# Performance work log

Measured on AMD Instinct MI355X. Metric: run time of the kernel, lower is better.

The kernel has to match this reference:

```python
import jax, jax.numpy as jnp
import numpy as np

HIDDEN = 1024
HEADS = 16
BATCH = 2
SEQ = 2048
# dropout_p = 0.1 but module evaluated in eval mode (training=False) -> identity


def setup_inputs() -> dict:
    key = jax.random.key(0)
    k1, k2, k3 = jax.random.split(key, 3)
    x = jax.random.normal(k1, (BATCH, SEQ, HIDDEN), dtype=jnp.float32)
    # unit-scaling Linear: weight ~ N(0,1) (reset_parameters uses nn.init.normal_)
    w_qkv = jax.random.normal(k2, (3 * HIDDEN, HIDDEN), dtype=jnp.float32)
    w_o = jax.random.normal(k3, (HIDDEN, HIDDEN), dtype=jnp.float32)
    return {"x": x, "w_qkv": w_qkv, "w_o": w_o}


def reference(x, w_qkv, w_o):
    b, s, hid = x.shape
    heads = HEADS
    d = hid // heads
    # unit-scaled linear (constraint='to_output_scale'): y = x @ W.T * fan_in**-0.5
    qkv = (x @ w_qkv.T) * (hid ** -0.5)            # [b, s, 3*hid]
    # einops 'b s (z h d) -> z b h s d'
    qkv = qkv.reshape(b, s, 3, heads, d)
    q = jnp.transpose(qkv[:, :, 0], (0, 2, 1, 3))   # [b, h, s, d]
    k = jnp.transpose(qkv[:, :, 1], (0, 2, 1, 3))
    v = jnp.transpose(qkv[:, :, 2], (0, 2, 1, 3))
    # unit-scaled matmul: scale = inner_dim**-0.5
    scores = jnp.einsum('bhqd,bhkd->bhqk', q, k) * (d ** -0.5)  # [b, h, s, s]
    # unit-scaled softmax: output_scale = n / sqrt(n - 1)
    attn = jax.nn.softmax(scores, axis=-1) * (s / np.sqrt(s - 1.0))
    # dropout inactive (eval mode)
    out = jnp.einsum('bhqk,bhkd->bhqd', attn, v) * (s ** -0.5)  # inner dim = s
    out = jnp.transpose(out, (0, 2, 1, 3)).reshape(b, s, hid)   # 'b h s d -> b s (h d)'
    return (out @ w_o.T) * (hid ** -0.5)
```

## Files before the change

### kernel.cpp

```cpp
#include <hip/hip_runtime.h>

typedef unsigned short u16;
typedef _Float16 f16x8 __attribute__((ext_vector_type(8)));
typedef _Float16 f16x4 __attribute__((ext_vector_type(4)));
typedef _Float16 f16x2 __attribute__((ext_vector_type(2)));
typedef float f32x4 __attribute__((ext_vector_type(4)));
typedef unsigned short u16x4 __attribute__((ext_vector_type(4)));

#define HID 1024
#define SEQ 2048
#define NH 16
#define DH 64

__device__ __forceinline__ u16 f2h(float f) {
  return __builtin_bit_cast(u16, (_Float16)f);
}
__device__ __forceinline__ f32x4 mfma_h(f16x8 a, f16x8 b, f32x4 c) {
  return __builtin_amdgcn_mfma_f32_16x16x32_f16(a, b, c, 0, 0, 0);
}
__device__ __forceinline__ float fexp2(float x) {
#if __has_builtin(__builtin_amdgcn_exp2f)
  return __builtin_amdgcn_exp2f(x);
#else
  return __expf(0.69314718f * x);
#endif
}
__device__ __forceinline__ f16x2 pkrtz(float a, float b) {
  return __builtin_bit_cast(f16x2, __builtin_amdgcn_cvt_pkrtz(a, b));
}
__device__ __forceinline__ void g2l16(const u16* g, u16* l) {
  __builtin_amdgcn_global_load_lds(
      (const __attribute__((address_space(1))) unsigned int*)g,
      (__attribute__((address_space(3))) unsigned int*)l, 16, 0, 0);
}

#define NX4 ((4096 * 1024) / 4)
#define NQ4 ((3072 * 1024) / 4)
#define NO4 ((1024 * 1024) / 4)
__global__ __launch_bounds__(256) void prep_kernel(
    const float* __restrict__ x, const float* __restrict__ wq,
    const float* __restrict__ wo,
    u16* __restrict__ x16, u16* __restrict__ wq16, u16* __restrict__ wo16) {
  int i = blockIdx.x * 256 + threadIdx.x;
  const float4 v = (i < NX4) ? ((const float4*)x)[i]
                 : (i < NX4 + NQ4) ? ((const float4*)wq)[i - NX4]
                 : ((const float4*)wo)[i - NX4 - NQ4];
  u16* dst = (i < NX4) ? &x16[(size_t)i * 4]
           : (i < NX4 + NQ4) ? &wq16[(size_t)(i - NX4) * 4]
           : &wo16[(size_t)(i - NX4 - NQ4) * 4];
  u16x4 o;
  o[0] = f2h(v.x); o[1] = f2h(v.y); o[2] = f2h(v.z); o[3] = f2h(v.w);
  *(u16x4*)dst = o;
}

__global__ __launch_bounds__(256, 3) void gemm_qkv(
    const u16* __restrict__ a16, const u16* __restrict__ b16,
    u16* __restrict__ qf, u16* __restrict__ kf, u16* __restrict__ vtf) {
  __shared__ __align__(16) u16 la[128 * 64], lb[128 * 64];
  const int t = threadIdx.x;
  const int lane = t & 63, w = t >> 6;
  const int wr = w >> 1, wc = w & 1;
  const int lr = lane & 15, lg = lane >> 4;
  const int br = blockIdx.x, bc = blockIdx.y;
  const f32x4 fzero = {0.f, 0.f, 0.f, 0.f};
  f32x4 acc[4][4];
#pragma unroll
  for (int i = 0; i < 4; ++i)
#pragma unroll
    for (int j = 0; j < 4; ++j) acc[i][j] = fzero;
  const int srow = t >> 3, scol = ((t & 7) ^ (srow & 7)) << 3;
  const u16* ga = a16 + (size_t)(br * 128 + srow) * HID + scol;
  const u16* gb = b16 + (size_t)(bc * 128 + srow) * HID + scol;
  const int lo16 = t * 8;
  for (int kk = 0; kk < HID; kk += 64) {
#pragma unroll
    for (int r = 0; r < 4; ++r)
      g2l16(ga + kk + (size_t)(r * 32) * HID, &la[lo16 + r * 2048]);
#pragma unroll
    for (int r = 0; r < 4; ++r)
      g2l16(gb + kk + (size_t)(r * 32) * HID, &lb[lo16 + r * 2048]);
    __syncthreads();
#pragma unroll
    for (int ks = 0; ks < 2; ++ks) {
      f16x8 ah[4], bh[4];
#pragma unroll
      for (int i = 0; i < 4; ++i) {
        int row = wr * 64 + i * 16 + lr;
        ah[i] = *(const f16x8*)&la[row * 64 + (((ks * 4 + lg) ^ (row & 7)) << 3)];
      }
#pragma unroll
      for (int j = 0; j < 4; ++j) {
        int row = wc * 64 + j * 16 + lr;
        bh[j] = *(const f16x8*)&lb[row * 64 + (((ks * 4 + lg) ^ (row & 7)) << 3)];
      }
#pragma unroll
      for (int i = 0; i < 4; ++i)
#pragma unroll
        for (int j = 0; j < 4; ++j) acc[i][j] = mfma_h(ah[i], bh[j], acc[i][j]);
    }
    __syncthreads();
  }
  const int m0 = br * 128 + wr * 64, n0 = bc * 128 + wc * 64;
#pragma unroll
  for (int i = 0; i < 4; ++i)
#pragma unroll
    for (int j = 0; j < 4; ++j)
#pragma unroll
      for (int r = 0; r < 4; ++r) {
        int row = m0 + i * 16 + lg * 4 + r;
        int col = n0 + j * 16 + lr;
        float val = acc[i][j][r] * 0.03125f;
        int b = row >> 11, s = row & 2047;
        int z = col >> 10, hh = (col >> 6) & 15, d = col & 63;
        int bhid = b * NH + hh;
        if (z == 0) {
          qf[((size_t)bhid * SEQ + s) * DH + d] = f2h(val * 0.18033688f);
        } else if (z == 1) {
          kf[((size_t)bhid * SEQ + s) * DH + d] = f2h(val);
        } else {
          int kv = s & 63;
          int ct = kv >> 4, lgv = (kv >> 2) & 3, rv = kv & 3;
          int kvp = ((ct >> 1) << 5) | (lgv << 3) | ((ct & 1) << 2) | rv;
          int s2 = (s & ~63) | kvp;
          vtf[((size_t)bhid * DH + d) * SEQ + s2] = f2h(val);
        }
      }
}

__global__ __launch_bounds__(256, 2) void gemm_proj(
    const u16* __restrict__ po0, const u16* __restrict__ po1,
    const float* __restrict__ pl, const u16* __restrict__ b16,
    float* __restrict__ out) {
  __shared__ __align__(16) u16 la[128 * 64];
  __shared__ __align__(16) u16 lb[64 * 64];
  __shared__ float linv[16 * 128];
  const int t = threadIdx.x;
  const int lane = t & 63, w = t >> 6;
  const int wr = w >> 1, wc = w & 1;
  const int lr = lane & 15, lg = lane >> 4;
  const int br = blockIdx.x, bc = blockIdx.y;
  const f32x4 fzero = {0.f, 0.f, 0.f, 0.f};
  f32x4 acc[4][2];
#pragma unroll
  for (int i = 0; i < 4; ++i)
#pragma unroll
    for (int j = 0; j < 2; ++j) acc[i][j] = fzero;
#pragma unroll
  for (int jj = 0; jj < 8; ++jj) {
    int idx = t + jj * 256;
    int h = idx >> 7, i = idx & 127;
    int ar = br * 128 + i;
    int b = ar >> 11, s = ar & 2047;
    int bhs = (b * NH + h) * SEQ + s;
    linv[idx] = 1.00024426f / (pl[bhs] + pl[NH * 2 * SEQ + bhs]);
  }
  __syncthreads();
  const int srow = t >> 3, scol = ((t & 7) ^ (srow & 7)) << 3;
  const u16* gp0 = po0 + (size_t)(br * 128 + srow) * HID + scol;
  const u16* gp1 = po1 + (size_t)(br * 128 + srow) * HID + scol;
  const u16* gb = b16 + (size_t)(bc * 64 + srow) * HID + scol;
  const int lo16 = t * 8;
  for (int kk = 0; kk < HID; kk += 64) {
#pragma unroll
    for (int r = 0; r < 2; ++r)
      g2l16(gb + kk + (size_t)(r * 32) * HID, &lb[lo16 + r * 2048]);
#pragma unroll
    for (int r = 0; r < 4; ++r) {
      f16x8 a0 = *(const f16x8*)(gp0 + kk + (size_t)(r * 32) * HID);
      f16x8 a1 = *(const f16x8*)(gp1 + kk + (size_t)(r * 32) * HID);
      float invr = linv[((kk >> 6) << 7) + srow + r * 32];
      union { f16x2 h2[4]; f16x8 h8; } uo;
#pragma unroll
      for (int p = 0; p < 4; ++p) {
        float s0 = ((float)a0[2 * p] + (float)a1[2 * p]) * invr;
        float s1 = ((float)a0[2 * p + 1] + (float)a1[2 * p + 1]) * invr;
        uo.h2[p] = pkrtz(s0, s1);
      }
      *(f16x8*)&la[lo16 + r * 2048] = uo.h8;
    }
    __syncthreads();
#pragma unroll
    for (int ks = 0; ks < 2; ++ks) {
      f16x8 ah[4], bh[2];
#pragma unroll
      for (int i = 0; i < 4; ++i) {
        int row = wr * 64 + i * 16 + lr;
        ah[i] = *(const f16x8*)&la[row * 64 + (((ks * 4 + lg) ^ (row & 7)) << 3)];
      }
#pragma unroll
      for (int j = 0; j < 2; ++j) {
        int row = wc * 32 + j * 16 + lr;
        bh[j] = *(const f16x8*)&lb[row * 64 + (((ks * 4 + lg) ^ (row & 7)) << 3)];
      }
#pragma unroll
      for (int i = 0; i < 4; ++i)
#pragma unroll
        for (int j = 0; j < 2; ++j)
          acc[i][j] = mfma_h(ah[i], bh[j], acc[i][j]);
    }
    __syncthreads();
  }
  const int m0 = br * 128 + wr * 64, n0 = bc * 64 + wc * 32;
#pragma unroll
  for (int i = 0; i < 4; ++i)
#pragma unroll
    for (int j = 0; j < 2; ++j)
#pragma unroll
      for (int r = 0; r < 4; ++r) {
        int row = m0 + i * 16 + lg * 4 + r;
        int col = n0 + j * 16 + lr;
        out[(size_t)row * HID + col] = acc[i][j][r] * 0.03125f;
      }
}

__global__ __launch_bounds__(256, 4) void attn_kernel(
    const u16* __restrict__ qf, const u16* __restrict__ kf,
    const u16* __restrict__ vtf, u16* __restrict__ po0,
    u16* __restrict__ po1, float* __restrict__ pl) {
  __shared__ __align__(16) u16 lk[2][64 * 64];
  __shared__ __align__(16) u16 lv[2][64 * 64];
  const int t = threadIdx.x;
  const int lane = t & 63, w = t >> 6;
  const int lr = lane & 15, lg = lane >> 4;
  const int bh = blockIdx.x, qt = blockIdx.y, sp = blockIdx.z;
  const size_t base_qk = (size_t)bh * SEQ * DH;
  const size_t base_vt = (size_t)bh * DH * SEQ;

  f16x8 qfr[2][2];
#pragma unroll
  for (int rt = 0; rt < 2; ++rt)
#pragma unroll
    for (int ks = 0; ks < 2; ++ks)
      qfr[rt][ks] = *(const f16x8*)&qf[base_qk +
          (size_t)(qt * 128 + w * 32 + rt * 16 + lr) * DH + ks * 32 + lg * 8];

  f16x8 vones;
#pragma unroll
  for (int j = 0; j < 8; ++j) vones[j] = (_Float16)1.0f;

  const f32x4 fzero = {0.f, 0.f, 0.f, 0.f};
  f32x4 acc_o[2][4];
  f32x4 acc_l[2];
#pragma unroll
  for (int rt = 0; rt < 2; ++rt) {
    acc_l[rt] = fzero;
#pragma unroll
    for (int ct = 0; ct < 4; ++ct) acc_o[rt][ct] = fzero;
  }

  const int srow = t >> 3;
  const int scol = ((t & 7) ^ (srow & 7)) << 3;
  const int lo16 = t * 8;

  const u16* gk0 = kf + base_qk + (size_t)(sp * 1024 + srow) * DH + scol;
  const u16* gv0 = vtf + base_vt + (size_t)srow * SEQ + sp * 1024 + scol;

#define STAGE(buf, j)                                             \
  {                                                               \
    const u16* gk = gk0 + (size_t)(j) * 64 * DH;                  \
    g2l16(gk, &lk[buf][lo16]);                                    \
    g2l16(gk + 32 * DH, &lk[buf][lo16 + 2048]);                   \
    const u16* gv = gv0 + (j) * 64;                               \
    g2l16(gv, &lv[buf][lo16]);                                    \
    g2l16(gv + (size_t)32 * SEQ, &lv[buf][lo16 + 2048]);          \
  }

  STAGE(0, 0)

  for (int j = 0; j < 16; ++j) {
    const int cur = j & 1;
    __syncthreads();

    f32x4 sa[2][4];
    __builtin_amdgcn_s_setprio(1);
#pragma unroll
    for (int ct = 0; ct < 4; ++ct) {
      int row = ct * 16 + lr;
      f16x8 k0 = *(const f16x8*)&lk[cur][row * 64 + ((lg ^ (row & 7)) << 3)];
      f16x8 k1 = *(const f16x8*)&lk[cur][row * 64 + (((4 + lg) ^ (row & 7)) << 3)];
      sa[0][ct] = mfma_h(k0, qfr[0][0], fzero);
      sa[1][ct] = mfma_h(k0, qfr[1][0], fzero);
      sa[0][ct] = mfma_h(k1, qfr[0][1], sa[0][ct]);
      sa[1][ct] = mfma_h(k1, qfr[1][1], sa[1][ct]);
    }
    __builtin_amdgcn_s_setprio(0);

    if (j + 1 < 16) STAGE(cur ^ 1, j + 1)

    f16x8 pfr[2][2];
#pragma unroll
    for (int rt = 0; rt < 2; ++rt)
#pragma unroll
      for (int ks = 0; ks < 2; ++ks) {
        union { f16x2 h2[4]; f16x8 h8; } up;
#pragma unroll
        for (int hi = 0; hi < 2; ++hi) {
          float e0 = fexp2(sa[rt][ks * 2 + hi][0]);
          float e1 = fexp2(sa[rt][ks * 2 + hi][1]);
          float e2 = fexp2(sa[rt][ks * 2 + hi][2]);
          float e3 = fexp2(sa[rt][ks * 2 + hi][3]);
          up.h2[hi * 2] = pkrtz(e0, e1);
          up.h2[hi * 2 + 1] = pkrtz(e2, e3);
        }
        pfr[rt][ks] = up.h8;
      }

    __builtin_amdgcn_s_setprio(1);
#pragma unroll
    for (int ks = 0; ks < 2; ++ks)
#pragma unroll
      for (int ct = 0; ct < 4; ++ct) {
        int vrow = ct * 16 + lr;
        f16x8 vfr = *(const f16x8*)&lv[cur][vrow * 64 + (((ks * 4 + lg) ^ (vrow & 7)) << 3)];
#pragma unroll
        for (int rt = 0; rt < 2; ++rt) acc_o[rt][ct] = mfma_h(pfr[rt][ks], vfr, acc_o[rt][ct]);
      }
#pragma unroll
    for (int rt = 0; rt < 2; ++rt) {
      acc_l[rt] = mfma_h(pfr[rt][0], vones, acc_l[rt]);
      acc_l[rt] = mfma_h(pfr[rt][1], vones, acc_l[rt]);
    }
    __builtin_amdgcn_s_setprio(0);
  }

  const int b = bh >> 4, hh = bh & 15;
  u16* pob = sp ? po1 : po0;
  float* plb = pl + sp * (NH * 2 * SEQ);
#pragma unroll
  for (int rt = 0; rt < 2; ++rt)
#pragma unroll
    for (int r = 0; r < 4; ++r) {
      int s = qt * 128 + w * 32 + rt * 16 + lg * 4 + r;
      int row = b * SEQ + s;
      if (lr == 0) plb[bh * SEQ + s] = acc_l[rt][r];
#pragma unroll
      for (int ct = 0; ct < 4; ++ct) {
        int d = ct * 16 + lr;
        pob[(size_t)row * HID + hh * DH + d] = f2h(acc_o[rt][ct][r]);
      }
    }
}

extern "C" void kernel_launch(void* const* d_in, const int* in_sizes, int n_in,
                              void* d_out, int out_size, void* d_ws, size_t ws_size,
                              hipStream_t stream) {
  const float* x = (const float*)d_in[0];
  const float* w_qkv = (const float*)d_in[1];
  const float* w_o = (const float*)d_in[2];
  u16* ws = (u16*)d_ws;
  const size_t XS = (size_t)4096 * 1024;
  const size_t WQ = (size_t)3072 * 1024;
  const size_t WO = (size_t)1024 * 1024;
  u16* x16  = ws;           u16* wq16 = x16 + XS;
  u16* wo16 = wq16 + WQ;
  u16* q_f  = wo16 + WO;    u16* k_f  = q_f + XS;
  u16* vt_f = k_f + XS;     u16* po0  = vt_f + XS;
  u16* po1  = x16;
  float* pl = (float*)wq16;

  prep_kernel<<<(NX4 + NQ4 + NO4) / 256, 256, 0, stream>>>(
      x, w_qkv, w_o, x16, wq16, wo16);
  gemm_qkv<<<dim3(32, 24), 256, 0, stream>>>(x16, wq16, q_f, k_f, vt_f);
  attn_kernel<<<dim3(32, 16, 2), 256, 0, stream>>>(q_f, k_f, vt_f, po0, po1, pl);
  gemm_proj<<<dim3(32, 16), 256, 0, stream>>>(po0, po1, pl, wo16, (float*)d_out);
}
```

Before: 178.6 us.

## Double-buffer QKV GEMM LDS tiles and vectorize V-transpose epilogue stores

The QKV projection GEMM now uses two 128x32 LDS buffers per operand and prefetches the next K-slice while computing the current one, with one barrier per iteration instead of two. The swizzle is adapted to the narrower 32-column tile. The epilogue hoists per-warp head/z decoding out of the inner loops and writes the permuted V-transpose layout with 4-wide vector stores. This aims to hide global-to-LDS latency and cut epilogue store overhead, at the cost of more loop iterations with smaller MFMA batches.

```diff
diff --git a/kernel.cpp b/kernel.cpp
--- a/kernel.cpp
+++ b/kernel.cpp
@@ -56,7 +56,7 @@
 __global__ __launch_bounds__(256, 3) void gemm_qkv(
     const u16* __restrict__ a16, const u16* __restrict__ b16,
     u16* __restrict__ qf, u16* __restrict__ kf, u16* __restrict__ vtf) {
-  __shared__ __align__(16) u16 la[128 * 64], lb[128 * 64];
+  __shared__ __align__(16) u16 la[2][128 * 32], lb[2][128 * 32];
   const int t = threadIdx.x;
   const int lane = t & 63, w = t >> 6;
   const int wr = w >> 1, wc = w & 1;
@@ -68,63 +68,76 @@
   for (int i = 0; i < 4; ++i)
 #pragma unroll
     for (int j = 0; j < 4; ++j) acc[i][j] = fzero;
-  const int srow = t >> 3, scol = ((t & 7) ^ (srow & 7)) << 3;
+  const int srow = t >> 2, scol = ((t & 3) ^ (srow & 3)) << 3;
   const u16* ga = a16 + (size_t)(br * 128 + srow) * HID + scol;
   const u16* gb = b16 + (size_t)(bc * 128 + srow) * HID + scol;
   const int lo16 = t * 8;
-  for (int kk = 0; kk < HID; kk += 64) {
-#pragma unroll
-    for (int r = 0; r < 4; ++r)
-      g2l16(ga + kk + (size_t)(r * 32) * HID, &la[lo16 + r * 2048]);
-#pragma unroll
-    for (int r = 0; r < 4; ++r)
-      g2l16(gb + kk + (size_t)(r * 32) * HID, &lb[lo16 + r * 2048]);
+
+#define QSTAGE(buf, s)                                        \
+  {                                                           \
+    const int kk = (s) * 32;                                  \
+    g2l16(ga + kk, &la[buf][lo16]);                           \
+    g2l16(ga + kk + (size_t)64 * HID, &la[buf][lo16 + 2048]); \
+    g2l16(gb + kk, &lb[buf][lo16]);                           \
+    g2l16(gb + kk + (size_t)64 * HID, &lb[buf][lo16 + 2048]); \
+  }
+
+  QSTAGE(0, 0)
+  for (int s = 0; s < 32; ++s) {
+    const int cur = s & 1;
     __syncthreads();
-#pragma unroll
-    for (int ks = 0; ks < 2; ++ks) {
-      f16x8 ah[4], bh[4];
-#pragma unroll
-      for (int i = 0; i < 4; ++i) {
-        int row = wr * 64 + i * 16 + lr;
-        ah[i] = *(const f16x8*)&la[row * 64 + (((ks * 4 + lg) ^ (row & 7)) << 3)];
-      }
+    if (s + 1 < 32) QSTAGE(cur ^ 1, s + 1)
+    f16x8 ah[4], bh[4];
+#pragma unroll
+    for (int i = 0; i < 4; ++i) {
+      int row = wr * 64 + i * 16 + lr;
+      ah[i] = *(const f16x8*)&la[cur][row * 32 + ((lg ^ (row & 3)) << 3)];
+    }
+#pragma unroll
+    for (int j = 0; j < 4; ++j) {
+      int row = wc * 64 + j * 16 + lr;
+      bh[j] = *(const f16x8*)&lb[cur][row * 32 + ((lg ^ (row & 3)) << 3)];
+    }
+#pragma unroll
+    for (int i = 0; i < 4; ++i)
+#pragma unroll
+      for (int j = 0; j < 4; ++j) acc[i][j] = mfma_h(ah[i], bh[j], acc[i][j]);
+  }
+#undef QSTAGE
+
+  const int m0 = br * 128 + wr * 64;
+  const int b = m0 >> 11, sbase = m0 & 2047;
+  const int hcol = bc * 2 + wc;
+  const int z = hcol >> 4, hh = hcol & 15;
+  const int bhid = b * NH + hh;
+  if (z == 2) {
+#pragma unroll
+    for (int i = 0; i < 4; ++i) {
+      int s2b = sbase + ((i >> 1) << 5) + (lg << 3) + ((i & 1) << 2);
 #pragma unroll
       for (int j = 0; j < 4; ++j) {
-        int row = wc * 64 + j * 16 + lr;
-        bh[j] = *(const f16x8*)&lb[row * 64 + (((ks * 4 + lg) ^ (row & 7)) << 3)];
-      }
-#pragma unroll
-      for (int i = 0; i < 4; ++i)
-#pragma unroll
-        for (int j = 0; j < 4; ++j) acc[i][j] = mfma_h(ah[i], bh[j], acc[i][j]);
-    }
-    __syncthreads();
-  }
-  const int m0 = br * 128 + wr * 64, n0 = bc * 128 + wc * 64;
-#pragma unroll
-  for (int i = 0; i < 4; ++i)
-#pragma unroll
-    for (int j = 0; j < 4; ++j)
-#pragma unroll
-      for (int r = 0; r < 4; ++r) {
-        int row = m0 + i * 16 + lg * 4 + r;
-        int col = n0 + j * 16 + lr;
-        float val = acc[i][j][r] * 0.03125f;
-        int b = row >> 11, s = row & 2047;
-        int z = col >> 10, hh = (col >> 6) & 15, d = col & 63;
-        int bhid = b * NH + hh;
-        if (z == 0) {
-          qf[((size_t)bhid * SEQ + s) * DH + d] = f2h(val * 0.18033688f);
-        } else if (z == 1) {
-          kf[((size_t)bhid * SEQ + s) * DH + d] = f2h(val);
-        } else {
-          int kv = s & 63;
-          int ct = kv >> 4, lgv = (kv >> 2) & 3, rv = kv & 3;
-          int kvp = ((ct >> 1) << 5) | (lgv << 3) | ((ct & 1) << 2) | rv;
-          int s2 = (s & ~63) | kvp;
-          vtf[((size_t)bhid * DH + d) * SEQ + s2] = f2h(val);
+        int d = j * 16 + lr;
+        u16x4 o;
+#pragma unroll
+        for (int r = 0; r < 4; ++r) o[r] = f2h(acc[i][j][r] * 0.03125f);
+        *(u16x4*)&vtf[((size_t)bhid * DH + d) * SEQ + s2b] = o;
+      }
+    }
+  } else {
+    const float sc = (z == 0) ? 0.03125f * 0.18033688f : 0.03125f;
+    u16* dst = (z == 0) ? qf : kf;
+#pragma unroll
+    for (int i = 0; i < 4; ++i)
+#pragma unroll
+      for (int j = 0; j < 4; ++j) {
+        int d = j * 16 + lr;
+#pragma unroll
+        for (int r = 0; r < 4; ++r) {
+          int ss = sbase + i * 16 + lg * 4 + r;
+          dst[((size_t)bhid * SEQ + ss) * DH + d] = f2h(acc[i][j][r] * sc);
         }
       }
+  }
 }
 
 __global__ __launch_bounds__(256, 2) void gemm_proj(
```

Result: slower. 183.8 us (+2.9%).
